# Performance work log

Hardware: AMD Instinct MI355X
Metric: run time of the kernel (lower is better)

Reference implementation:

```python
import jax, jax.numpy as jnp
import numpy as np

W1_XYZ, W2_XYZ, W3_XYZ = 0.3, 0.3, 1.0
W1_WPQR, W2_WPQR, W3_WPQR = 150.0, 150.0, 500.0
EPS = 1e-12  # F.normalize eps
B = 1048576


def setup_inputs() -> dict:
    key = jax.random.key(0)
    ks = jax.random.split(key, 7)
    return {
        "p1_xyz": jax.random.normal(ks[0], (B, 3), dtype=jnp.float32),
        "p1_wpqr": jax.random.normal(ks[1], (B, 4), dtype=jnp.float32),
        "p2_xyz": jax.random.normal(ks[2], (B, 3), dtype=jnp.float32),
        "p2_wpqr": jax.random.normal(ks[3], (B, 4), dtype=jnp.float32),
        "p3_xyz": jax.random.normal(ks[4], (B, 3), dtype=jnp.float32),
        "p3_wpqr": jax.random.normal(ks[5], (B, 4), dtype=jnp.float32),
        "poseGT": jax.random.normal(ks[6], (B, 7), dtype=jnp.float32),
    }


def _l2(x):  # row-wise L2 norm, [B, d] -> [B]
    return jnp.sqrt(jnp.sum(x * x, axis=-1))


def reference(p1_xyz, p1_wpqr, p2_xyz, p2_wpqr, p3_xyz, p3_wpqr, poseGT):
    p_gt = poseGT[:, :3]                     # [B,3]
    q_gt = poseGT[:, 3:]                     # [B,4]
    q_gtn = q_gt / jnp.maximum(_l2(q_gt), EPS)[:, None]  # F.normalize(p=2)

    loss1 = _l2(p1_xyz - p_gt) + W1_WPQR * _l2(p1_wpqr - q_gtn)
    loss2 = _l2(p2_xyz - p_gt) + W2_WPQR * _l2(p2_wpqr - q_gtn)
    loss3 = _l2(p3_xyz - p_gt) + W3_WPQR * _l2(p3_wpqr - q_gtn)

    per_sample = W1_XYZ * loss1 + W2_XYZ * loss2 + W3_XYZ * loss3  # [B]
    return jnp.sum(per_sample) / p_gt.shape[0]
```

## Files before the change

kernel.cpp:

```cpp
#include <hip/hip_runtime.h>


#define W1_XYZ 0.3f
#define W2_XYZ 0.3f
#define W3_XYZ 1.0f
#define W1_WPQR 150.0f
#define W2_WPQR 150.0f
#define W3_WPQR 500.0f
#define EPSF 1e-12f

constexpr int B_TOTAL = 1048576;
constexpr int SPT = 2;
constexpr int BLOCK = 256;
constexpr int NBLOCKS = B_TOTAL / (SPT * BLOCK);

__global__ __launch_bounds__(BLOCK) void pose_loss_partial(
    const float* __restrict__ p1x, const float* __restrict__ p1q,
    const float* __restrict__ p2x, const float* __restrict__ p2q,
    const float* __restrict__ p3x, const float* __restrict__ p3q,
    const float* __restrict__ gt, float* __restrict__ partial)
{
    const long t = (long)blockIdx.x * BLOCK + threadIdx.x;

    __attribute__((aligned(8))) float x1[6], x2[6], x3[6];
    __attribute__((aligned(8))) float q1[8], q2[8], q3[8];
    __attribute__((aligned(8))) float g[14];

    {
        const float2* v;
        v = reinterpret_cast<const float2*>(p1x) + 3 * t;
        #pragma unroll
        for (int i = 0; i < 3; ++i) reinterpret_cast<float2*>(x1)[i] = v[i];
        v = reinterpret_cast<const float2*>(p2x) + 3 * t;
        #pragma unroll
        for (int i = 0; i < 3; ++i) reinterpret_cast<float2*>(x2)[i] = v[i];
        v = reinterpret_cast<const float2*>(p3x) + 3 * t;
        #pragma unroll
        for (int i = 0; i < 3; ++i) reinterpret_cast<float2*>(x3)[i] = v[i];
        v = reinterpret_cast<const float2*>(p1q) + 4 * t;
        #pragma unroll
        for (int i = 0; i < 4; ++i) reinterpret_cast<float2*>(q1)[i] = v[i];
        v = reinterpret_cast<const float2*>(p2q) + 4 * t;
        #pragma unroll
        for (int i = 0; i < 4; ++i) reinterpret_cast<float2*>(q2)[i] = v[i];
        v = reinterpret_cast<const float2*>(p3q) + 4 * t;
        #pragma unroll
        for (int i = 0; i < 4; ++i) reinterpret_cast<float2*>(q3)[i] = v[i];
        v = reinterpret_cast<const float2*>(gt) + 7 * t;
        #pragma unroll
        for (int i = 0; i < 7; ++i) reinterpret_cast<float2*>(g)[i] = v[i];
    }

    float acc = 0.0f;
    #pragma unroll
    for (int j = 0; j < SPT; ++j) {
        const float px = g[7*j+0], py = g[7*j+1], pz = g[7*j+2];
        float qa = g[7*j+3], qb = g[7*j+4], qc = g[7*j+5], qd = g[7*j+6];
        const float qn = sqrtf(qa*qa + qb*qb + qc*qc + qd*qd);
        const float inv = 1.0f / fmaxf(qn, EPSF);
        qa *= inv; qb *= inv; qc *= inv; qd *= inv;

        float dx, dy, dz, dw;

        dx = x1[3*j+0] - px; dy = x1[3*j+1] - py; dz = x1[3*j+2] - pz;
        const float l1x = sqrtf(dx*dx + dy*dy + dz*dz);
        dw = q1[4*j+0] - qa; dx = q1[4*j+1] - qb; dy = q1[4*j+2] - qc; dz = q1[4*j+3] - qd;
        const float l1q = sqrtf(dw*dw + dx*dx + dy*dy + dz*dz);

        dx = x2[3*j+0] - px; dy = x2[3*j+1] - py; dz = x2[3*j+2] - pz;
        const float l2x = sqrtf(dx*dx + dy*dy + dz*dz);
        dw = q2[4*j+0] - qa; dx = q2[4*j+1] - qb; dy = q2[4*j+2] - qc; dz = q2[4*j+3] - qd;
        const float l2q = sqrtf(dw*dw + dx*dx + dy*dy + dz*dz);

        dx = x3[3*j+0] - px; dy = x3[3*j+1] - py; dz = x3[3*j+2] - pz;
        const float l3x = sqrtf(dx*dx + dy*dy + dz*dz);
        dw = q3[4*j+0] - qa; dx = q3[4*j+1] - qb; dy = q3[4*j+2] - qc; dz = q3[4*j+3] - qd;
        const float l3q = sqrtf(dw*dw + dx*dx + dy*dy + dz*dz);

        acc += W1_XYZ * (l1x + W1_WPQR * l1q)
             + W2_XYZ * (l2x + W2_WPQR * l2q)
             + W3_XYZ * (l3x + W3_WPQR * l3q);
    }

    #pragma unroll
    for (int off = 32; off > 0; off >>= 1)
        acc += __shfl_down(acc, off);

    __shared__ float smem[BLOCK / 64];
    const int wid = threadIdx.x >> 6;
    if ((threadIdx.x & 63) == 0) smem[wid] = acc;
    __syncthreads();
    if (threadIdx.x == 0) {
        float s = 0.0f;
        #pragma unroll
        for (int w = 0; w < BLOCK / 64; ++w) s += smem[w];
        partial[blockIdx.x] = s;
    }
}

__global__ __launch_bounds__(BLOCK) void pose_loss_final(
    const float* __restrict__ partial, float* __restrict__ out, int n, float scale)
{
    float acc = 0.0f;
    for (int i = threadIdx.x; i < n; i += BLOCK) acc += partial[i];

    #pragma unroll
    for (int off = 32; off > 0; off >>= 1)
        acc += __shfl_down(acc, off);

    __shared__ float smem[BLOCK / 64];
    const int wid = threadIdx.x >> 6;
    if ((threadIdx.x & 63) == 0) smem[wid] = acc;
    __syncthreads();
    if (threadIdx.x == 0) {
        float s = 0.0f;
        #pragma unroll
        for (int w = 0; w < BLOCK / 64; ++w) s += smem[w];
        out[0] = s * scale;
    }
}

extern "C" void kernel_launch(void* const* d_in, const int* in_sizes, int n_in,
                              void* d_out, int out_size, void* d_ws, size_t ws_size,
                              hipStream_t stream) {
    const float* p1x = (const float*)d_in[0];
    const float* p1q = (const float*)d_in[1];
    const float* p2x = (const float*)d_in[2];
    const float* p2q = (const float*)d_in[3];
    const float* p3x = (const float*)d_in[4];
    const float* p3q = (const float*)d_in[5];
    const float* gt  = (const float*)d_in[6];
    float* out = (float*)d_out;
    float* partial = (float*)d_ws;

    pose_loss_partial<<<NBLOCKS, BLOCK, 0, stream>>>(p1x, p1q, p2x, p2q, p3x, p3q, gt, partial);
    pose_loss_final<<<1, BLOCK, 0, stream>>>(partial, out, NBLOCKS, 1.0f / (float)B_TOTAL);
}
```

Measured before the change: 27.22 us.

## Stage block inputs into LDS via direct global-to-LDS 16-byte loads

Each block now covers 256 samples, one per thread, instead of two per thread. The four waves each issue 16-byte global_load_lds transfers that copy contiguous slices of every input array straight into shared memory, and threads then read their sample's fields from LDS after a barrier. This replaces strided 8-byte per-thread loads with fully coalesced wide loads. In exchange it adds a block-wide barrier, 28 KB of LDS per block that can limit occupancy, twice as many blocks, and strided LDS reads that may hit bank conflicts.

```diff
diff --git a/kernel.cpp b/kernel.cpp
--- a/kernel.cpp
+++ b/kernel.cpp
@@ -10,9 +10,18 @@
 #define EPSF 1e-12f
 
 constexpr int B_TOTAL = 1048576;
-constexpr int SPT = 2;
 constexpr int BLOCK = 256;
-constexpr int NBLOCKS = B_TOTAL / (SPT * BLOCK);
+constexpr int SPB = 256;
+constexpr int NBLOCKS = B_TOTAL / SPB;
+
+#define X1O 0
+#define X2O 768
+#define X3O 1536
+#define Q1O 2304
+#define Q2O 3328
+#define Q3O 4352
+#define GO  5376
+#define LDSF 7168
 
 __global__ __launch_bounds__(BLOCK) void pose_loss_partial(
     const float* __restrict__ p1x, const float* __restrict__ p1q,
@@ -20,81 +29,104 @@
     const float* __restrict__ p3x, const float* __restrict__ p3q,
     const float* __restrict__ gt, float* __restrict__ partial)
 {
-    const long t = (long)blockIdx.x * BLOCK + threadIdx.x;
+    __shared__ float lds[LDSF];
+    const int tid  = threadIdx.x;
+    const int wid  = tid >> 6;
+    const int lane = tid & 63;
+    const long blk = blockIdx.x;
 
-    __attribute__((aligned(8))) float x1[6], x2[6], x3[6];
-    __attribute__((aligned(8))) float q1[8], q2[8], q3[8];
-    __attribute__((aligned(8))) float g[14];
+    const char* bx1 = (const char*)p1x + blk * 3072 + (long)lane * 16;
+    const char* bx2 = (const char*)p2x + blk * 3072 + (long)lane * 16;
+    const char* bx3 = (const char*)p3x + blk * 3072 + (long)lane * 16;
+    const char* bq1 = (const char*)p1q + blk * 4096 + (long)lane * 16;
+    const char* bq2 = (const char*)p2q + blk * 4096 + (long)lane * 16;
+    const char* bq3 = (const char*)p3q + blk * 4096 + (long)lane * 16;
+    const char* bg  = (const char*)gt  + blk * 7168 + (long)lane * 16;
+    char* l = (char*)lds;
 
-    {
-        const float2* v;
-        v = reinterpret_cast<const float2*>(p1x) + 3 * t;
-        #pragma unroll
-        for (int i = 0; i < 3; ++i) reinterpret_cast<float2*>(x1)[i] = v[i];
-        v = reinterpret_cast<const float2*>(p2x) + 3 * t;
-        #pragma unroll
-        for (int i = 0; i < 3; ++i) reinterpret_cast<float2*>(x2)[i] = v[i];
-        v = reinterpret_cast<const float2*>(p3x) + 3 * t;
-        #pragma unroll
-        for (int i = 0; i < 3; ++i) reinterpret_cast<float2*>(x3)[i] = v[i];
-        v = reinterpret_cast<const float2*>(p1q) + 4 * t;
-        #pragma unroll
-        for (int i = 0; i < 4; ++i) reinterpret_cast<float2*>(q1)[i] = v[i];
-        v = reinterpret_cast<const float2*>(p2q) + 4 * t;
-        #pragma unroll
-        for (int i = 0; i < 4; ++i) reinterpret_cast<float2*>(q2)[i] = v[i];
-        v = reinterpret_cast<const float2*>(p3q) + 4 * t;
-        #pragma unroll
-        for (int i = 0; i < 4; ++i) reinterpret_cast<float2*>(q3)[i] = v[i];
-        v = reinterpret_cast<const float2*>(gt) + 7 * t;
-        #pragma unroll
-        for (int i = 0; i < 7; ++i) reinterpret_cast<float2*>(g)[i] = v[i];
+    if (wid == 0) {
+        __builtin_amdgcn_global_load_lds((const void*)(bx1 +    0), (void*)(l + X1O*4 +    0), 16, 0, 0);
+        __builtin_amdgcn_global_load_lds((const void*)(bx1 + 1024), (void*)(l + X1O*4 + 1024), 16, 0, 0);
+        __builtin_amdgcn_global_load_lds((const void*)(bx1 + 2048), (void*)(l + X1O*4 + 2048), 16, 0, 0);
+        __builtin_amdgcn_global_load_lds((const void*)(bg  +    0), (void*)(l + GO*4  +    0), 16, 0, 0);
+        __builtin_amdgcn_global_load_lds((const void*)(bg  + 1024), (void*)(l + GO*4  + 1024), 16, 0, 0);
+        __builtin_amdgcn_global_load_lds((const void*)(bg  + 2048), (void*)(l + GO*4  + 2048), 16, 0, 0);
+        __builtin_amdgcn_global_load_lds((const void*)(bg  + 3072), (void*)(l + GO*4  + 3072), 16, 0, 0);
+    } else if (wid == 1) {
+        __builtin_amdgcn_global_load_lds((const void*)(bx2 +    0), (void*)(l + X2O*4 +    0), 16, 0, 0);
+        __builtin_amdgcn_global_load_lds((const void*)(bx2 + 1024), (void*)(l + X2O*4 + 1024), 16, 0, 0);
+        __builtin_amdgcn_global_load_lds((const void*)(bx2 + 2048), (void*)(l + X2O*4 + 2048), 16, 0, 0);
+        __builtin_amdgcn_global_load_lds((const void*)(bq1 +    0), (void*)(l + Q1O*4 +    0), 16, 0, 0);
+        __builtin_amdgcn_global_load_lds((const void*)(bq1 + 1024), (void*)(l + Q1O*4 + 1024), 16, 0, 0);
+        __builtin_amdgcn_global_load_lds((const void*)(bq1 + 2048), (void*)(l + Q1O*4 + 2048), 16, 0, 0);
+        __builtin_amdgcn_global_load_lds((const void*)(bq1 + 3072), (void*)(l + Q1O*4 + 3072), 16, 0, 0);
+    } else if (wid == 2) {
+        __builtin_amdgcn_global_load_lds((const void*)(bx3 +    0), (void*)(l + X3O*4 +    0), 16, 0, 0);
+        __builtin_amdgcn_global_load_lds((const void*)(bx3 + 1024), (void*)(l + X3O*4 + 1024), 16, 0, 0);
+        __builtin_amdgcn_global_load_lds((const void*)(bx3 + 2048), (void*)(l + X3O*4 + 2048), 16, 0, 0);
+        __builtin_amdgcn_global_load_lds((const void*)(bq2 +    0), (void*)(l + Q2O*4 +    0), 16, 0, 0);
+        __builtin_amdgcn_global_load_lds((const void*)(bq2 + 1024), (void*)(l + Q2O*4 + 1024), 16, 0, 0);
+        __builtin_amdgcn_global_load_lds((const void*)(bq2 + 2048), (void*)(l + Q2O*4 + 2048), 16, 0, 0);
+        __builtin_amdgcn_global_load_lds((const void*)(bq2 + 3072), (void*)(l + Q2O*4 + 3072), 16, 0, 0);
+    } else {
+        __builtin_amdgcn_global_load_lds((const void*)(bg  + 4096), (void*)(l + GO*4  + 4096), 16, 0, 0);
+        __builtin_amdgcn_global_load_lds((const void*)(bg  + 5120), (void*)(l + GO*4  + 5120), 16, 0, 0);
+        __builtin_amdgcn_global_load_lds((const void*)(bg  + 6144), (void*)(l + GO*4  + 6144), 16, 0, 0);
+        __builtin_amdgcn_global_load_lds((const void*)(bq3 +    0), (void*)(l + Q3O*4 +    0), 16, 0, 0);
+        __builtin_amdgcn_global_load_lds((const void*)(bq3 + 1024), (void*)(l + Q3O*4 + 1024), 16, 0, 0);
+        __builtin_amdgcn_global_load_lds((const void*)(bq3 + 2048), (void*)(l + Q3O*4 + 2048), 16, 0, 0);
+        __builtin_amdgcn_global_load_lds((const void*)(bq3 + 3072), (void*)(l + Q3O*4 + 3072), 16, 0, 0);
     }
+    __syncthreads();
 
-    float acc = 0.0f;
-    #pragma unroll
-    for (int j = 0; j < SPT; ++j) {
-        const float px = g[7*j+0], py = g[7*j+1], pz = g[7*j+2];
-        float qa = g[7*j+3], qb = g[7*j+4], qc = g[7*j+5], qd = g[7*j+6];
-        const float qn = sqrtf(qa*qa + qb*qb + qc*qc + qd*qd);
-        const float inv = 1.0f / fmaxf(qn, EPSF);
-        qa *= inv; qb *= inv; qc *= inv; qd *= inv;
+    const int s = tid;
+    const float px = lds[GO + 7*s + 0];
+    const float py = lds[GO + 7*s + 1];
+    const float pz = lds[GO + 7*s + 2];
+    float qa = lds[GO + 7*s + 3];
+    float qb = lds[GO + 7*s + 4];
+    float qc = lds[GO + 7*s + 5];
+    float qd = lds[GO + 7*s + 6];
+    const float qn  = sqrtf(qa*qa + qb*qb + qc*qc + qd*qd);
+    const float inv = 1.0f / fmaxf(qn, EPSF);
+    qa *= inv; qb *= inv; qc *= inv; qd *= inv;
 
-        float dx, dy, dz, dw;
+    float dx, dy, dz, dw;
 
-        dx = x1[3*j+0] - px; dy = x1[3*j+1] - py; dz = x1[3*j+2] - pz;
-        const float l1x = sqrtf(dx*dx + dy*dy + dz*dz);
-        dw = q1[4*j+0] - qa; dx = q1[4*j+1] - qb; dy = q1[4*j+2] - qc; dz = q1[4*j+3] - qd;
-        const float l1q = sqrtf(dw*dw + dx*dx + dy*dy + dz*dz);
+    dx = lds[X1O + 3*s + 0] - px; dy = lds[X1O + 3*s + 1] - py; dz = lds[X1O + 3*s + 2] - pz;
+    const float l1x = sqrtf(dx*dx + dy*dy + dz*dz);
+    dw = lds[Q1O + 4*s + 0] - qa; dx = lds[Q1O + 4*s + 1] - qb;
+    dy = lds[Q1O + 4*s + 2] - qc; dz = lds[Q1O + 4*s + 3] - qd;
+    const float l1q = sqrtf(dw*dw + dx*dx + dy*dy + dz*dz);
 
-        dx = x2[3*j+0] - px; dy = x2[3*j+1] - py; dz = x2[3*j+2] - pz;
-        const float l2x = sqrtf(dx*dx + dy*dy + dz*dz);
-        dw = q2[4*j+0] - qa; dx = q2[4*j+1] - qb; dy = q2[4*j+2] - qc; dz = q2[4*j+3] - qd;
-        const float l2q = sqrtf(dw*dw + dx*dx + dy*dy + dz*dz);
+    dx = lds[X2O + 3*s + 0] - px; dy = lds[X2O + 3*s + 1] - py; dz = lds[X2O + 3*s + 2] - pz;
+    const float l2x = sqrtf(dx*dx + dy*dy + dz*dz);
+    dw = lds[Q2O + 4*s + 0] - qa; dx = lds[Q2O + 4*s + 1] - qb;
+    dy = lds[Q2O + 4*s + 2] - qc; dz = lds[Q2O + 4*s + 3] - qd;
+    const float l2q = sqrtf(dw*dw + dx*dx + dy*dy + dz*dz);
 
-        dx = x3[3*j+0] - px; dy = x3[3*j+1] - py; dz = x3[3*j+2] - pz;
-        const float l3x = sqrtf(dx*dx + dy*dy + dz*dz);
-        dw = q3[4*j+0] - qa; dx = q3[4*j+1] - qb; dy = q3[4*j+2] - qc; dz = q3[4*j+3] - qd;
-        const float l3q = sqrtf(dw*dw + dx*dx + dy*dy + dz*dz);
+    dx = lds[X3O + 3*s + 0] - px; dy = lds[X3O + 3*s + 1] - py; dz = lds[X3O + 3*s + 2] - pz;
+    const float l3x = sqrtf(dx*dx + dy*dy + dz*dz);
+    dw = lds[Q3O + 4*s + 0] - qa; dx = lds[Q3O + 4*s + 1] - qb;
+    dy = lds[Q3O + 4*s + 2] - qc; dz = lds[Q3O + 4*s + 3] - qd;
+    const float l3q = sqrtf(dw*dw + dx*dx + dy*dy + dz*dz);
 
-        acc += W1_XYZ * (l1x + W1_WPQR * l1q)
-             + W2_XYZ * (l2x + W2_WPQR * l2q)
-             + W3_XYZ * (l3x + W3_WPQR * l3q);
-    }
+    float acc = W1_XYZ * (l1x + W1_WPQR * l1q)
+              + W2_XYZ * (l2x + W2_WPQR * l2q)
+              + W3_XYZ * (l3x + W3_WPQR * l3q);
 
     #pragma unroll
     for (int off = 32; off > 0; off >>= 1)
         acc += __shfl_down(acc, off);
 
-    __shared__ float smem[BLOCK / 64];
-    const int wid = threadIdx.x >> 6;
-    if ((threadIdx.x & 63) == 0) smem[wid] = acc;
+    __shared__ float red[BLOCK / 64];
+    if ((tid & 63) == 0) red[wid] = acc;
     __syncthreads();
-    if (threadIdx.x == 0) {
-        float s = 0.0f;
+    if (tid == 0) {
+        float ssum = 0.0f;
         #pragma unroll
-        for (int w = 0; w < BLOCK / 64; ++w) s += smem[w];
-        partial[blockIdx.x] = s;
+        for (int w = 0; w < BLOCK / 64; ++w) ssum += red[w];
+        partial[blk] = ssum;
     }
 }
 
```

Measured after the change: 28.18 us. 3.5% more time.

## Stage AoS inputs through LDS with coalesced float4 loads, per-wave partials

Applied to the files above, without the earlier changes.

Each wave now handles 256 samples, loading the xyz and poseGT arrays as fully coalesced float4 vectors into LDS, then reading strided per-sample values back from LDS. Quaternion inputs are loaded directly as float4 per sample. Normalization uses a hardware rsq clamped at 1e12, and the sqrt calls become the raw hardware sqrt. The block-level reduction is replaced by one partial per wave, and the final kernel sums 4096 partials with 1024 threads. The aim is wider, coalesced global loads; the cost is 64KB of LDS per block, which limits occupancy, and slightly less exact sqrt and rsq results.

```diff
diff --git a/kernel.cpp b/kernel.cpp
--- a/kernel.cpp
+++ b/kernel.cpp
@@ -7,12 +7,15 @@
 #define W1_WPQR 150.0f
 #define W2_WPQR 150.0f
 #define W3_WPQR 500.0f
-#define EPSF 1e-12f
 
 constexpr int B_TOTAL = 1048576;
-constexpr int SPT = 2;
 constexpr int BLOCK = 256;
-constexpr int NBLOCKS = B_TOTAL / (SPT * BLOCK);
+constexpr int WPB = 4;
+constexpr int SPW = 256;
+constexpr int NBLOCKS = B_TOTAL / (WPB * SPW);
+constexpr int NWAVES  = NBLOCKS * WPB;
+
+constexpr int WAVE_LDS_BYTES = 16384;
 
 __global__ __launch_bounds__(BLOCK) void pose_loss_partial(
     const float* __restrict__ p1x, const float* __restrict__ p1q,
@@ -20,62 +23,83 @@
     const float* __restrict__ p3x, const float* __restrict__ p3q,
     const float* __restrict__ gt, float* __restrict__ partial)
 {
-    const long t = (long)blockIdx.x * BLOCK + threadIdx.x;
+    __shared__ __align__(16) char lds[WPB * WAVE_LDS_BYTES];
+    const int tid  = threadIdx.x;
+    const int wid  = tid >> 6;
+    const int lane = tid & 63;
+    const long W   = (long)blockIdx.x * WPB + wid;
 
-    __attribute__((aligned(8))) float x1[6], x2[6], x3[6];
-    __attribute__((aligned(8))) float q1[8], q2[8], q3[8];
-    __attribute__((aligned(8))) float g[14];
+    float* Lx1 = (float*)(lds + wid * WAVE_LDS_BYTES);
+    float* Lx2 = Lx1 + 768;
+    float* Lx3 = Lx1 + 1536;
+    float* Lg  = Lx1 + 2304;
 
-    {
-        const float2* v;
-        v = reinterpret_cast<const float2*>(p1x) + 3 * t;
-        #pragma unroll
-        for (int i = 0; i < 3; ++i) reinterpret_cast<float2*>(x1)[i] = v[i];
-        v = reinterpret_cast<const float2*>(p2x) + 3 * t;
-        #pragma unroll
-        for (int i = 0; i < 3; ++i) reinterpret_cast<float2*>(x2)[i] = v[i];
-        v = reinterpret_cast<const float2*>(p3x) + 3 * t;
-        #pragma unroll
-        for (int i = 0; i < 3; ++i) reinterpret_cast<float2*>(x3)[i] = v[i];
-        v = reinterpret_cast<const float2*>(p1q) + 4 * t;
-        #pragma unroll
-        for (int i = 0; i < 4; ++i) reinterpret_cast<float2*>(q1)[i] = v[i];
-        v = reinterpret_cast<const float2*>(p2q) + 4 * t;
-        #pragma unroll
-        for (int i = 0; i < 4; ++i) reinterpret_cast<float2*>(q2)[i] = v[i];
-        v = reinterpret_cast<const float2*>(p3q) + 4 * t;
-        #pragma unroll
-        for (int i = 0; i < 4; ++i) reinterpret_cast<float2*>(q3)[i] = v[i];
-        v = reinterpret_cast<const float2*>(gt) + 7 * t;
-        #pragma unroll
-        for (int i = 0; i < 7; ++i) reinterpret_cast<float2*>(g)[i] = v[i];
+    const float4* q1p = (const float4*)p1q;
+    const float4* q2p = (const float4*)p2q;
+    const float4* q3p = (const float4*)p3q;
+    float4 q1v[4], q2v[4], q3v[4];
+    #pragma unroll
+    for (int k = 0; k < 4; ++k) {
+        const long s = W * SPW + (long)(k * 64 + lane);
+        q1v[k] = q1p[s];
+        q2v[k] = q2p[s];
+        q3v[k] = q3p[s];
     }
+
+    const float4* x1p = (const float4*)p1x;
+    const float4* x2p = (const float4*)p2x;
+    const float4* x3p = (const float4*)p3x;
+    const float4* gp  = (const float4*)gt;
+    float4 xs1[3], xs2[3], xs3[3], gs[7];
+    #pragma unroll
+    for (int j = 0; j < 3; ++j) xs1[j] = x1p[W * 192 + (long)(j * 64 + lane)];
+    #pragma unroll
+    for (int j = 0; j < 3; ++j) xs2[j] = x2p[W * 192 + (long)(j * 64 + lane)];
+    #pragma unroll
+    for (int j = 0; j < 3; ++j) xs3[j] = x3p[W * 192 + (long)(j * 64 + lane)];
+    #pragma unroll
+    for (int j = 0; j < 7; ++j) gs[j]  = gp [W * 448 + (long)(j * 64 + lane)];
+
+    #pragma unroll
+    for (int j = 0; j < 3; ++j) ((float4*)Lx1)[j * 64 + lane] = xs1[j];
+    #pragma unroll
+    for (int j = 0; j < 3; ++j) ((float4*)Lx2)[j * 64 + lane] = xs2[j];
+    #pragma unroll
+    for (int j = 0; j < 3; ++j) ((float4*)Lx3)[j * 64 + lane] = xs3[j];
+    #pragma unroll
+    for (int j = 0; j < 7; ++j) ((float4*)Lg )[j * 64 + lane] = gs[j];
 
     float acc = 0.0f;
     #pragma unroll
-    for (int j = 0; j < SPT; ++j) {
-        const float px = g[7*j+0], py = g[7*j+1], pz = g[7*j+2];
-        float qa = g[7*j+3], qb = g[7*j+4], qc = g[7*j+5], qd = g[7*j+6];
-        const float qn = sqrtf(qa*qa + qb*qb + qc*qc + qd*qd);
-        const float inv = 1.0f / fmaxf(qn, EPSF);
-        qa *= inv; qb *= inv; qc *= inv; qd *= inv;
+    for (int k = 0; k < 4; ++k) {
+        const int s = k * 64 + lane;
+        const float px = Lg[7*s + 0];
+        const float py = Lg[7*s + 1];
+        const float pz = Lg[7*s + 2];
+        const float qa0 = Lg[7*s + 3];
+        const float qb0 = Lg[7*s + 4];
+        const float qc0 = Lg[7*s + 5];
+        const float qd0 = Lg[7*s + 6];
+        const float d   = qa0*qa0 + qb0*qb0 + qc0*qc0 + qd0*qd0;
+        const float inv = fminf(__builtin_amdgcn_rsqf(d), 1e12f);
+        const float qa = qa0 * inv, qb = qb0 * inv, qc = qc0 * inv, qd = qd0 * inv;
 
         float dx, dy, dz, dw;
 
-        dx = x1[3*j+0] - px; dy = x1[3*j+1] - py; dz = x1[3*j+2] - pz;
-        const float l1x = sqrtf(dx*dx + dy*dy + dz*dz);
-        dw = q1[4*j+0] - qa; dx = q1[4*j+1] - qb; dy = q1[4*j+2] - qc; dz = q1[4*j+3] - qd;
-        const float l1q = sqrtf(dw*dw + dx*dx + dy*dy + dz*dz);
+        dx = Lx1[3*s + 0] - px; dy = Lx1[3*s + 1] - py; dz = Lx1[3*s + 2] - pz;
+        const float l1x = __builtin_amdgcn_sqrtf(dx*dx + dy*dy + dz*dz);
+        dw = q1v[k].x - qa; dx = q1v[k].y - qb; dy = q1v[k].z - qc; dz = q1v[k].w - qd;
+        const float l1q = __builtin_amdgcn_sqrtf(dw*dw + dx*dx + dy*dy + dz*dz);
 
-        dx = x2[3*j+0] - px; dy = x2[3*j+1] - py; dz = x2[3*j+2] - pz;
-        const float l2x = sqrtf(dx*dx + dy*dy + dz*dz);
-        dw = q2[4*j+0] - qa; dx = q2[4*j+1] - qb; dy = q2[4*j+2] - qc; dz = q2[4*j+3] - qd;
-        const float l2q = sqrtf(dw*dw + dx*dx + dy*dy + dz*dz);
+        dx = Lx2[3*s + 0] - px; dy = Lx2[3*s + 1] - py; dz = Lx2[3*s + 2] - pz;
+        const float l2x = __builtin_amdgcn_sqrtf(dx*dx + dy*dy + dz*dz);
+        dw = q2v[k].x - qa; dx = q2v[k].y - qb; dy = q2v[k].z - qc; dz = q2v[k].w - qd;
+        const float l2q = __builtin_amdgcn_sqrtf(dw*dw + dx*dx + dy*dy + dz*dz);
 
-        dx = x3[3*j+0] - px; dy = x3[3*j+1] - py; dz = x3[3*j+2] - pz;
-        const float l3x = sqrtf(dx*dx + dy*dy + dz*dz);
-        dw = q3[4*j+0] - qa; dx = q3[4*j+1] - qb; dy = q3[4*j+2] - qc; dz = q3[4*j+3] - qd;
-        const float l3q = sqrtf(dw*dw + dx*dx + dy*dy + dz*dz);
+        dx = Lx3[3*s + 0] - px; dy = Lx3[3*s + 1] - py; dz = Lx3[3*s + 2] - pz;
+        const float l3x = __builtin_amdgcn_sqrtf(dx*dx + dy*dy + dz*dz);
+        dw = q3v[k].x - qa; dx = q3v[k].y - qb; dy = q3v[k].z - qc; dz = q3v[k].w - qd;
+        const float l3q = __builtin_amdgcn_sqrtf(dw*dw + dx*dx + dy*dy + dz*dz);
 
         acc += W1_XYZ * (l1x + W1_WPQR * l1q)
              + W2_XYZ * (l2x + W2_WPQR * l2q)
@@ -85,37 +109,27 @@
     #pragma unroll
     for (int off = 32; off > 0; off >>= 1)
         acc += __shfl_down(acc, off);
-
-    __shared__ float smem[BLOCK / 64];
-    const int wid = threadIdx.x >> 6;
-    if ((threadIdx.x & 63) == 0) smem[wid] = acc;
-    __syncthreads();
-    if (threadIdx.x == 0) {
-        float s = 0.0f;
-        #pragma unroll
-        for (int w = 0; w < BLOCK / 64; ++w) s += smem[w];
-        partial[blockIdx.x] = s;
-    }
+    if (lane == 0) partial[W] = acc;
 }
 
-__global__ __launch_bounds__(BLOCK) void pose_loss_final(
-    const float* __restrict__ partial, float* __restrict__ out, int n, float scale)
+__global__ __launch_bounds__(1024) void pose_loss_final(
+    const float* __restrict__ partial, float* __restrict__ out, float scale)
 {
-    float acc = 0.0f;
-    for (int i = threadIdx.x; i < n; i += BLOCK) acc += partial[i];
+    const int tid = threadIdx.x;
+    const float4 v = ((const float4*)partial)[tid];
+    float acc = (v.x + v.y) + (v.z + v.w);
 
     #pragma unroll
     for (int off = 32; off > 0; off >>= 1)
         acc += __shfl_down(acc, off);
 
-    __shared__ float smem[BLOCK / 64];
-    const int wid = threadIdx.x >> 6;
-    if ((threadIdx.x & 63) == 0) smem[wid] = acc;
+    __shared__ float smem[16];
+    if ((tid & 63) == 0) smem[tid >> 6] = acc;
     __syncthreads();
-    if (threadIdx.x == 0) {
+    if (tid == 0) {
         float s = 0.0f;
         #pragma unroll
-        for (int w = 0; w < BLOCK / 64; ++w) s += smem[w];
+        for (int w = 0; w < 16; ++w) s += smem[w];
         out[0] = s * scale;
     }
 }
@@ -134,5 +148,5 @@
     float* partial = (float*)d_ws;
 
     pose_loss_partial<<<NBLOCKS, BLOCK, 0, stream>>>(p1x, p1q, p2x, p2q, p3x, p3q, gt, partial);
-    pose_loss_final<<<1, BLOCK, 0, stream>>>(partial, out, NBLOCKS, 1.0f / (float)B_TOTAL);
+    pose_loss_final<<<1, 1024, 0, stream>>>(partial, out, 1.0f / (float)B_TOTAL);
 }
```

Result: faster. 24.53 us (-9.9%).
